# Kernel tuning notes

Measured on AMD Instinct MI355X. Metric: run time of the kernel, lower is better.

The kernel has to match this reference:

```python
import jax, jax.numpy as jnp
import numpy as np

EPS = 1e-8
H, DH = 4, 8
HID = H * DH  # 32
FF = 20       # 4 * dim
C = 5         # channels per degree


def snorm(x):
    # grad-safe L2 norm over last axis
    return jnp.sqrt(jnp.sum(x * x, axis=-1) + 1e-12)


def _ln(v, gamma, beta):
    mu = v.mean(-1, keepdims=True)
    sd = v.std(-1, keepdims=True) + EPS
    return (v - mu) / sd * gamma + beta


def norm_se3(x0, x1, g, b):
    # equivariant norm: transform per-channel invariant norms, keep orientation (phase)
    n0 = jnp.abs(x0)
    y0 = jnp.sign(x0) * jax.nn.gelu(_ln(n0, g[0], b[0]))
    n1 = snorm(x1)                                        # (b,n,c)
    y1 = x1 / n1[..., None] * jax.nn.gelu(_ln(n1, g[1], b[1]))[..., None]
    return y0, y1


def attention(x0, x1, coors, adjm, Wq, Mk, Mv, R1, rb1, R2, rb2, Wo0, Wo1):
    b, n, c = x0.shape
    rel = coors[:, None, :, :] - coors[:, :, None, :]     # (b,i,j,3): x_j - x_i
    dist = jnp.sqrt(jnp.sum(rel * rel, -1, keepdims=True) + 1e-12)
    u = rel / dist                                        # unit directions
    # radial net -> per-edge kernel coefficients for each degree-pair/basis (k and v)
    phi = jax.nn.relu(dist @ R1 + rb1) @ R2 + rb2         # (b,i,j,12*HID)
    (k00, k10, k01, kI, kU, kX, v00, v10, v01, vI, vU, vX) = jnp.split(phi, 12, -1)

    def edge_feats(M, p00, p10, p01, pI, pU, pX):
        y00 = jnp.einsum('bjc,ch->bjh', x0, M[0])
        y10 = jnp.einsum('bjcm,ch->bjhm', x1, M[1])
        y01 = jnp.einsum('bjc,ch->bjh', x0, M[2])
        yI = jnp.einsum('bjcm,ch->bjhm', x1, M[3])
        yU = jnp.einsum('bjcm,ch->bjhm', x1, M[4])
        yX = jnp.einsum('bjcm,ch->bjhm', x1, M[5])
        # degree-0 messages: (0->0) scalar and (1->0) vector.dot(u) paths
        e0 = p00 * y00[:, None] + p10 * jnp.einsum('bjhm,bijm->bijh', y10, u)
        un = u[:, :, :, None, :]                          # (b,i,j,1,3)
        # degree-1 messages: closed-form equivariant bases u*s, I, u(u.v), u x v
        e1 = (p01[..., None] * y01[:, None, :, :, None] * un
              + pI[..., None] * yI[:, None]
              + pU[..., None] * jnp.einsum('bjhm,bijm->bijh', yU, u)[..., None] * un
              + pX[..., None] * jnp.cross(un, yX[:, None]))
        return e0, e1

    k0, k1 = edge_feats(Mk, k00, k10, k01, kI, kU, kX)
    v0, v1 = edge_feats(Mv, v00, v10, v01, vI, vU, vX)

    q0 = jnp.einsum('bic,ch->bih', x0, Wq[0]).reshape(b, n, H, DH)
    q1 = jnp.einsum('bicm,ch->bihm', x1, Wq[1]).reshape(b, n, H, DH, 3)
    logits = (jnp.einsum('bihd,bijhd->bhij', q0, k0.reshape(b, n, n, H, DH))
              + jnp.einsum('bihdm,bijhdm->bhij', q1, k1.reshape(b, n, n, H, DH, 3)))
    logits = logits / jnp.asarray(DH, x0.dtype) ** 0.5
    logits = jnp.where(adjm[:, None], logits, -1e9)       # sparse-neighbor mask
    attn = jax.nn.softmax(logits, axis=-1)
    o0 = jnp.einsum('bhij,bijhd->bihd', attn, v0.reshape(b, n, n, H, DH)).reshape(b, n, HID)
    o1 = jnp.einsum('bhij,bijhdm->bihdm', attn, v1.reshape(b, n, n, H, DH, 3)).reshape(b, n, HID, 3)
    return o0 @ Wo0, jnp.einsum('bnhm,hc->bncm', o1, Wo1)


def feedforward(x0, x1, Wf1, Wf2, gs, bs):
    h0 = jax.nn.gelu(jnp.einsum('bnc,cf->bnf', x0, Wf1[0]))
    h1 = jnp.einsum('bncm,cf->bnfm', x1, Wf1[1])
    h1 = h1 * jax.nn.sigmoid(snorm(h1) * gs + bs)[..., None]   # norm-gated nonlin (equivariant)
    return jnp.einsum('bnf,fc->bnc', h0, Wf2[0]), jnp.einsum('bnfm,fc->bncm', h1, Wf2[1])


def _forward(feats, coors, adj_mat, Wq, Mk, Mv, R1, rb1, R2, rb2, Wo0, Wo1, gnA, bnA, gnF, bnF, Wf1, Wf2, gs, bs, Wh1, bh1, Wh2, bh2):
    b, n, _ = feats.shape
    a = adj_mat.astype(jnp.float32)
    # num_adj_degrees=2: attend over 1-hop OR 2-hop neighbors (plus self)
    adjm = adj_mat | ((a @ a) > 0) | jnp.eye(n, dtype=bool)
    x0 = feats
    x1 = jnp.zeros(feats.shape + (3,), feats.dtype)       # input fiber has only degree-0
    x0n, x1n = norm_se3(x0, x1, gnA, bnA)
    d0, d1 = attention(x0n, x1n, coors, adjm, Wq, Mk, Mv, R1, rb1, R2, rb2, Wo0, Wo1)
    x0, x1 = x0 + d0, x1 + d1
    x0n, x1n = norm_se3(x0, x1, gnF, bnF)
    f0, f1 = feedforward(x0n, x1n, Wf1, Wf2, gs, bs)
    x0, x1 = x0 + f0, x1 + f1
    pooled = x0.mean(axis=1)                              # mean pool type-0 features
    h = jax.nn.relu(pooled @ Wh1 + bh1)
    out = h @ Wh2 + bh2                                   # (b, 9)
    return out.reshape(-1, 3, 3)


def setup_inputs():
    key = jax.random.key(0)
    ks = jax.random.split(key, 16)
    B, N = 2, 256
    g = lambda i, shape, s: jax.random.normal(ks[i], shape, jnp.float32) * s
    feats = g(0, (B, N, C), 1.0)
    coors = g(1, (B, N, 3), 3.0)
    r = jax.random.uniform(ks[2], (B, N, N))
    adj = r < 0.03
    adj = (adj | jnp.swapaxes(adj, 1, 2)) & ~jnp.eye(N, dtype=bool)
    s5, sh, sf, s128 = C ** -0.5, HID ** -0.5, FF ** -0.5, 128 ** -0.5
    return dict(
        feats=feats, coors=coors, adj_mat=adj,
        Wq=g(3, (2, C, HID), s5), Mk=g(4, (6, C, HID), s5), Mv=g(5, (6, C, HID), s5),
        R1=g(6, (1, 32), 1.0), rb1=jnp.zeros(32), R2=g(7, (32, 12 * HID), 32 ** -0.5), rb2=jnp.zeros(12 * HID),
        Wo0=g(8, (HID, C), sh), Wo1=g(9, (HID, C), sh),
        gnA=jnp.ones((2, C)), bnA=jnp.zeros((2, C)), gnF=jnp.ones((2, C)), bnF=jnp.zeros((2, C)),
        Wf1=g(10, (2, C, FF), s5), Wf2=g(11, (2, FF, C), sf), gs=jnp.ones(FF), bs=jnp.zeros(FF),
        Wh1=g(12, (C, 128), s5), bh1=jnp.zeros(128), Wh2=g(13, (128, 9), s128), bh2=jnp.zeros(9))


def reference(feats, coors, adj_mat, Wq, Mk, Mv, R1, rb1, R2, rb2, Wo0, Wo1, gnA, bnA, gnF, bnF, Wf1, Wf2, gs, bs, Wh1, bh1, Wh2, bh2):
    return _forward(feats, coors, adj_mat, Wq, Mk, Mv, R1, rb1, R2, rb2, Wo0, Wo1, gnA, bnA, gnF, bnF, Wf1, Wf2, gs, bs, Wh1, bh1, Wh2, bh2)
```

## Files before the change

### kernel.cpp

```cpp
#include <hip/hip_runtime.h>
#include <math.h>

#define NN 256
#define CC 5
#define HIDD 32


__device__ __forceinline__ float gelu_tanh(float x) {
    float x3 = x * x * x;
    return 0.5f * x * (1.0f + tanhf(0.7978845608028654f * (x + 0.044715f * x3)));
}
__device__ __forceinline__ float sgnf(float x) {
    return (x > 0.f) ? 1.f : ((x < 0.f) ? -1.f : 0.f);
}

#define TROW 9
#define TSZ (33 * TROW)

__global__ __launch_bounds__(256) void fused_attn(
    const float* __restrict__ coors,
    const int* __restrict__ adj,
    const float* __restrict__ feats,
    const float* __restrict__ Wq0, const float* __restrict__ Mk0, const float* __restrict__ Mv0,
    const float* __restrict__ gnA0, const float* __restrict__ bnA0,
    const float* __restrict__ R1, const float* __restrict__ rb1,
    const float* __restrict__ R2, const float* __restrict__ rb2,
    const float* __restrict__ Wo0,
    const float* __restrict__ gnF0, const float* __restrict__ bnF0,
    const float* __restrict__ Wf10,
    const float* __restrict__ Wf20,
    float* __restrict__ xfin)
{
    int node = blockIdx.x;
    int b = node >> 8, i = node & 255;
    int tid = threadIdx.x;
    int j = tid;
    int lane = tid & 63, wave = tid >> 6;

    __shared__ float4 sT[4 * TSZ];
    __shared__ float2 kv[32][32];
    __shared__ float2 srr[32];
    __shared__ float srb2k[32], srb2v[32];
    __shared__ float tt[32], sts[32];
    __shared__ unsigned int smask[33];
    __shared__ float q0s[32];
    __shared__ float Wo0t[5][32];
    __shared__ int nlist[NN];
    __shared__ int ncnt;
    __shared__ float wredm[4][4], wreds[4][4];
    __shared__ float ew[4][5], x0as[5], xfs[5], h0s[20];

    int av = adj[(size_t)(b * NN + i) * NN + j];

    for (int idx = tid; idx < 1024; idx += 256) {
        int w = idx >> 5, hd = idx & 31;
        kv[w][hd] = make_float2(R2[w * 384 + hd], R2[w * 384 + 192 + hd]);
    }
    if (tid < 32) {
        srr[tid] = make_float2(R1[tid], rb1[tid]);
        srb2k[tid] = rb2[tid];
        srb2v[tid] = rb2[192 + tid];
    }
    if (tid < 160) Wo0t[tid / 32][tid % 32] = Wo0[(tid % 32) * 5 + tid / 32];
    if (tid == 0) ncnt = 0;

    float dx = coors[(b * NN + j) * 3 + 0] - coors[(b * NN + i) * 3 + 0];
    float dy = coors[(b * NN + j) * 3 + 1] - coors[(b * NN + i) * 3 + 1];
    float dz = coors[(b * NN + j) * 3 + 2] - coors[(b * NN + i) * 3 + 2];
    float dist = sqrtf(dx * dx + dy * dy + dz * dz + 1e-12f);

    float x0n[CC];
    {
        const float* f = feats + (size_t)(b * NN + j) * CC;
        float fv[CC], n0[CC];
        float mu = 0.f;
#pragma unroll
        for (int c = 0; c < CC; c++) { fv[c] = f[c]; n0[c] = fabsf(fv[c]); mu += n0[c]; }
        mu *= (1.0f / CC);
        float var = 0.f;
#pragma unroll
        for (int c = 0; c < CC; c++) { float d = n0[c] - mu; var += d * d; }
        var *= (1.0f / CC);
        float sd = sqrtf(var) + 1e-8f;
#pragma unroll
        for (int c = 0; c < CC; c++) {
            float ln = (n0[c] - mu) / sd * gnA0[c] + bnA0[c];
            x0n[c] = sgnf(fv[c]) * gelu_tanh(ln);
        }
    }
    __syncthreads();

    if (tid < 32) {
        float r = srr[tid].x;
        tt[tid] = (r != 0.f) ? (-srr[tid].y / r) : -3.0e38f;
    }
    if (tid < 32) {
        float t = tt[tid];
        int rank = 0;
        for (int k = 0; k < 32; k++) {
            float tk = tt[k];
            rank += (tk < t) || (tk == t && k < tid);
        }
        sts[rank] = t;
    }
    if (tid < 33) {
        float rep = (tid == 0) ? (sts[0] - 1.0f)
                  : (tid == 32) ? (sts[31] + 1.0f)
                  : 0.5f * (sts[tid - 1] + sts[tid]);
        unsigned int m = 0;
        for (int w = 0; w < 32; w++) {
            float2 rr = srr[w];
            if (fmaf(rr.x, rep, rr.y) > 0.f) m |= (1u << w);
        }
        smask[tid] = m;
    }
    if (tid < 32) {
        const float* f = feats + (size_t)(b * NN + i) * CC;
        float fv[CC], n0[CC], xi[CC];
        float mu = 0.f;
#pragma unroll
        for (int c = 0; c < CC; c++) { fv[c] = f[c]; n0[c] = fabsf(fv[c]); mu += n0[c]; }
        mu *= (1.0f / CC);
        float var = 0.f;
#pragma unroll
        for (int c = 0; c < CC; c++) { float d = n0[c] - mu; var += d * d; }
        var *= (1.0f / CC);
        float sd = sqrtf(var) + 1e-8f;
#pragma unroll
        for (int c = 0; c < CC; c++) {
            float ln = (n0[c] - mu) / sd * gnA0[c] + bnA0[c];
            xi[c] = sgnf(fv[c]) * gelu_tanh(ln);
        }
        float q = 0.f;
#pragma unroll
        for (int c = 0; c < CC; c++) q = fmaf(xi[c], Wq0[c * HIDD + tid], q);
        q0s[tid] = q;
    }
    if (av) { int p = atomicAdd(&ncnt, 1); nlist[p] = j; }

    float ykr[32];
#pragma unroll
    for (int hd = 0; hd < 32; hd++) ykr[hd] = 0.f;
#pragma unroll
    for (int c = 0; c < CC; c++) {
        float xc = x0n[c];
#pragma unroll
        for (int hd = 0; hd < 32; hd++)
            ykr[hd] = fmaf(xc, Mk0[c * HIDD + hd], ykr[hd]);
    }
    __syncthreads();

    int okacc = (av != 0) || (i == j);
    {
        int cnt = ncnt;
        for (int t = 0; t < cnt; t += 8) {
            int idxs[8], vv[8];
#pragma unroll
            for (int k = 0; k < 8; k++) {
                int u = t + k;
                idxs[k] = nlist[(u < cnt) ? u : t];
            }
#pragma unroll
            for (int k = 0; k < 8; k++)
                vv[k] = adj[(size_t)(b * NN + idxs[k]) * NN + j];
#pragma unroll
            for (int k = 0; k < 8; k++) okacc |= vv[k];
        }
    }
    for (int idx = tid; idx < 33 * 32; idx += 256) {
        int p = idx >> 5, hd = idx & 31;
        unsigned int m = smask[p];
        float A = 0.f, Bv = 0.f, Cv = 0.f, Dv = 0.f;
        while (m) {
            int w = __ffs(m) - 1;
            m &= (m - 1);
            float2 rr = srr[w];
            float2 kw = kv[w][hd];
            A  = fmaf(rr.x, kw.x, A);  Bv = fmaf(rr.y, kw.x, Bv);
            Cv = fmaf(rr.x, kw.y, Cv); Dv = fmaf(rr.y, kw.y, Dv);
        }
        Bv += srb2k[hd];
        Dv += srb2v[hd];
        float* tf = (float*)sT;
        tf[(0 * TSZ + p * TROW) * 4 + hd] = A;
        tf[(1 * TSZ + p * TROW) * 4 + hd] = Bv;
        tf[(2 * TSZ + p * TROW) * 4 + hd] = Cv;
        tf[(3 * TSZ + p * TROW) * 4 + hd] = Dv;
    }
    __syncthreads();

    int p = 0;
#pragma unroll
    for (int k = 0; k < 32; k++) p += (sts[k] < dist) ? 1 : 0;

    const float4* Ap = sT + 0 * TSZ + p * TROW;
    const float4* Bp = sT + 1 * TSZ + p * TROW;
    const float4* Cp = sT + 2 * TSZ + p * TROW;
    const float4* Dp = sT + 3 * TSZ + p * TROW;
    const float4* q04 = (const float4*)q0s;

    float lg[4] = {0.f, 0.f, 0.f, 0.f};
#pragma unroll
    for (int q = 0; q < 8; q++) {
        float4 a = Ap[q], bb = Bp[q], qq = q04[q];
        int h = q >> 1;
        lg[h] = fmaf(fmaf(dist, a.x, bb.x) * qq.x, ykr[4 * q + 0], lg[h]);
        lg[h] = fmaf(fmaf(dist, a.y, bb.y) * qq.y, ykr[4 * q + 1], lg[h]);
        lg[h] = fmaf(fmaf(dist, a.z, bb.z) * qq.z, ykr[4 * q + 2], lg[h]);
        lg[h] = fmaf(fmaf(dist, a.w, bb.w) * qq.w, ykr[4 * q + 3], lg[h]);
    }
    {
        const float invs = 0.35355339059327379f;
        bool ok = okacc != 0;
#pragma unroll
        for (int h = 0; h < 4; h++) lg[h] = ok ? lg[h] * invs : -1e9f;
    }

    float attn[4];
#pragma unroll
    for (int h = 0; h < 4; h++) {
        float v = lg[h];
        for (int off = 32; off; off >>= 1) v = fmaxf(v, __shfl_xor(v, off, 64));
        if (lane == 0) wredm[h][wave] = v;
    }
    __syncthreads();
    float hmv[4];
#pragma unroll
    for (int h = 0; h < 4; h++)
        hmv[h] = fmaxf(fmaxf(wredm[h][0], wredm[h][1]), fmaxf(wredm[h][2], wredm[h][3]));
#pragma unroll
    for (int h = 0; h < 4; h++) lg[h] = expf(lg[h] - hmv[h]);
#pragma unroll
    for (int h = 0; h < 4; h++) {
        float v = lg[h];
        for (int off = 32; off; off >>= 1) v += __shfl_xor(v, off, 64);
        if (lane == 0) wreds[h][wave] = v;
    }
    __syncthreads();
#pragma unroll
    for (int h = 0; h < 4; h++) {
        float hsv = wreds[h][0] + wreds[h][1] + wreds[h][2] + wreds[h][3];
        attn[h] = lg[h] / hsv;
    }

    float yvr[32];
#pragma unroll
    for (int hd = 0; hd < 32; hd++) yvr[hd] = 0.f;
#pragma unroll
    for (int c = 0; c < CC; c++) {
        float xc = x0n[c];
#pragma unroll
        for (int hd = 0; hd < 32; hd++)
            yvr[hd] = fmaf(xc, Mv0[c * HIDD + hd], yvr[hd]);
    }

    float e[5] = {0.f, 0.f, 0.f, 0.f, 0.f};
#pragma unroll
    for (int q = 0; q < 8; q++) {
        float4 c4 = Cp[q], d4 = Dp[q];
        float at = attn[q >> 1];
        float4 pv;
        pv.x = at * fmaf(dist, c4.x, d4.x) * yvr[4 * q + 0];
        pv.y = at * fmaf(dist, c4.y, d4.y) * yvr[4 * q + 1];
        pv.z = at * fmaf(dist, c4.z, d4.z) * yvr[4 * q + 2];
        pv.w = at * fmaf(dist, c4.w, d4.w) * yvr[4 * q + 3];
#pragma unroll
        for (int c = 0; c < 5; c++) {
            float4 w4 = ((const float4*)Wo0t[c])[q];
            e[c] = fmaf(pv.x, w4.x, fmaf(pv.y, w4.y, fmaf(pv.z, w4.z, fmaf(pv.w, w4.w, e[c]))));
        }
    }
    for (int off = 32; off; off >>= 1)
#pragma unroll
        for (int c = 0; c < 5; c++) e[c] += __shfl_xor(e[c], off, 64);
    if (lane == 0)
#pragma unroll
        for (int c = 0; c < 5; c++) ew[wave][c] = e[c];
    __syncthreads();

    if (wave != 0) return;

    if (lane < 5) {
        float d0 = ew[0][lane] + ew[1][lane] + ew[2][lane] + ew[3][lane];
        x0as[lane] = feats[node * 5 + lane] + d0;
    }
    if (lane < 5) {
        float x0a[5], n0[5];
        float mu = 0.f;
#pragma unroll
        for (int c = 0; c < 5; c++) { x0a[c] = x0as[c]; n0[c] = fabsf(x0a[c]); mu += n0[c]; }
        mu *= 0.2f;
        float var = 0.f;
#pragma unroll
        for (int c = 0; c < 5; c++) { float d = n0[c] - mu; var += d * d; }
        var *= 0.2f;
        float sd = sqrtf(var) + 1e-8f;
        float ln = (n0[lane] - mu) / sd * gnF0[lane] + bnF0[lane];
        xfs[lane] = sgnf(x0a[lane]) * gelu_tanh(ln);
    }
    if (lane < 20) {
        float s = 0.f;
#pragma unroll
        for (int c = 0; c < 5; c++) s = fmaf(xfs[c], Wf10[c * 20 + lane], s);
        h0s[lane] = gelu_tanh(s);
    }
    if (lane < 5) {
        float f0 = 0.f;
        for (int f = 0; f < 20; f++) f0 = fmaf(h0s[f], Wf20[f * 5 + lane], f0);
        xfin[node * 5 + lane] = x0as[lane] + f0;
    }
}

__global__ __launch_bounds__(256) void head_mlp(const float* __restrict__ xfin,
                         const float* __restrict__ Wh1, const float* __restrict__ bh1,
                         const float* __restrict__ Wh2, const float* __restrict__ bh2,
                         float* __restrict__ out) {
    __shared__ float part[2][5][25];
    __shared__ float pooled[10];
    __shared__ float hdn[2][128];
    int tid = threadIdx.x;
    if (tid < 250) {
        int b = tid / 125, r = tid % 125, c = r / 25, grp = r % 25;
        float s = 0.f;
        for (int i = grp; i < NN; i += 25) s += xfin[(b * NN + i) * 5 + c];
        part[b][c][grp] = s;
    }
    __syncthreads();
    if (tid < 10) {
        int b = tid / 5, c = tid % 5;
        float s = 0.f;
        for (int g = 0; g < 25; g++) s += part[b][c][g];
        pooled[tid] = s * (1.0f / NN);
    }
    __syncthreads();
    {
        int b = tid >> 7, k = tid & 127;
        float s = bh1[k];
#pragma unroll
        for (int c = 0; c < 5; c++) s = fmaf(pooled[b * 5 + c], Wh1[c * 128 + k], s);
        hdn[b][k] = fmaxf(s, 0.f);
    }
    __syncthreads();
    if (tid < 18) {
        int b = tid / 9, o = tid % 9;
        float s = bh2[o];
        for (int k = 0; k < 128; k++) s = fmaf(hdn[b][k], Wh2[k * 9 + o], s);
        out[b * 9 + o] = s;
    }
}

extern "C" void kernel_launch(void* const* d_in, const int* in_sizes, int n_in,
                              void* d_out, int out_size, void* d_ws, size_t ws_size,
                              hipStream_t stream) {
    const float* feats = (const float*)d_in[0];
    const float* coors = (const float*)d_in[1];
    const int*   adj   = (const int*)d_in[2];
    const float* Wq    = (const float*)d_in[3];
    const float* Mk    = (const float*)d_in[4];
    const float* Mv    = (const float*)d_in[5];
    const float* R1    = (const float*)d_in[6];
    const float* rb1   = (const float*)d_in[7];
    const float* R2    = (const float*)d_in[8];
    const float* rb2   = (const float*)d_in[9];
    const float* Wo0   = (const float*)d_in[10];
    const float* gnA   = (const float*)d_in[12];
    const float* bnA   = (const float*)d_in[13];
    const float* gnF   = (const float*)d_in[14];
    const float* bnF   = (const float*)d_in[15];
    const float* Wf1   = (const float*)d_in[16];
    const float* Wf2   = (const float*)d_in[17];
    const float* Wh1   = (const float*)d_in[20];
    const float* bh1   = (const float*)d_in[21];
    const float* Wh2   = (const float*)d_in[22];
    const float* bh2   = (const float*)d_in[23];
    float* out = (float*)d_out;

    float* xfin = (float*)d_ws;

    hipLaunchKernelGGL(fused_attn, dim3(512), dim3(256), 0, stream,
                       coors, adj, feats, Wq, Mk, Mv, gnA, bnA, R1, rb1, R2, rb2,
                       Wo0, gnF, bnF, Wf1, Wf2, xfin);
    hipLaunchKernelGGL(head_mlp, dim3(1), dim3(256), 0, stream,
                       xfin, Wh1, bh1, Wh2, bh2, out);
}
```

Before: 125.3 us.

## Replace shared atomic neighbor list with ballot compaction and prefetch tail weights

The neighbor list is now built with per-wave ballot/popcount compaction instead of a shared-memory atomicAdd, which removes the counter initialisation and one block barrier. The adjacency gather loop is unrolled 16 wide and maps indices across the four per-wave segments. Weights used by the per-node FFN tail are prefetched into registers early, and the head MLP stages Wh2 in shared memory. The aim is to cut atomic serialisation and barrier and latency stalls, at the cost of more registers and extra index arithmetic.

```diff
diff --git a/kernel.cpp b/kernel.cpp
--- a/kernel.cpp
+++ b/kernel.cpp
@@ -46,7 +46,7 @@
     __shared__ float q0s[32];
     __shared__ float Wo0t[5][32];
     __shared__ int nlist[NN];
-    __shared__ int ncnt;
+    __shared__ int wcnt[4];
     __shared__ float wredm[4][4], wreds[4][4];
     __shared__ float ew[4][5], x0as[5], xfs[5], h0s[20];
 
@@ -62,7 +62,6 @@
         srb2v[tid] = rb2[192 + tid];
     }
     if (tid < 160) Wo0t[tid / 32][tid % 32] = Wo0[(tid % 32) * 5 + tid / 32];
-    if (tid == 0) ncnt = 0;
 
     float dx = coors[(b * NN + j) * 3 + 0] - coors[(b * NN + i) * 3 + 0];
     float dy = coors[(b * NN + j) * 3 + 1] - coors[(b * NN + i) * 3 + 1];
@@ -88,7 +87,6 @@
             x0n[c] = sgnf(fv[c]) * gelu_tanh(ln);
         }
     }
-    __syncthreads();
 
     if (tid < 32) {
         float r = srr[tid].x;
@@ -136,7 +134,29 @@
         for (int c = 0; c < CC; c++) q = fmaf(xi[c], Wq0[c * HIDD + tid], q);
         q0s[tid] = q;
     }
-    if (av) { int p = atomicAdd(&ncnt, 1); nlist[p] = j; }
+
+    float pfeat = 0.f, pgnF = 0.f, pbnF = 0.f;
+    float pWf1[CC], pWf2[20];
+    if (wave == 0) {
+        if (lane < 5) {
+            pfeat = feats[node * 5 + lane];
+            pgnF = gnF0[lane];
+            pbnF = bnF0[lane];
+#pragma unroll
+            for (int f = 0; f < 20; f++) pWf2[f] = Wf20[f * 5 + lane];
+        }
+        if (lane < 20) {
+#pragma unroll
+            for (int c = 0; c < CC; c++) pWf1[c] = Wf10[c * 20 + lane];
+        }
+    }
+
+    {
+        unsigned long long bm = __ballot(av != 0);
+        int pos = __popcll(bm & ((1ull << lane) - 1ull));
+        if (av) nlist[(wave << 6) + pos] = j;
+        if (lane == 0) wcnt[wave] = (int)__popcll(bm);
+    }
 
     float ykr[32];
 #pragma unroll
@@ -152,19 +172,26 @@
 
     int okacc = (av != 0) || (i == j);
     {
-        int cnt = ncnt;
-        for (int t = 0; t < cnt; t += 8) {
-            int idxs[8], vv[8];
-#pragma unroll
-            for (int k = 0; k < 8; k++) {
-                int u = t + k;
-                idxs[k] = nlist[(u < cnt) ? u : t];
+        int o1 = wcnt[0];
+        int o2 = o1 + wcnt[1];
+        int o3 = o2 + wcnt[2];
+        int total = o3 + wcnt[3];
+        for (int t0 = 0; t0 < total; t0 += 16) {
+            int idxs[16], vv[16];
+#pragma unroll
+            for (int k = 0; k < 16; k++) {
+                int u = t0 + k;
+                if (u >= total) u = t0;
+                int base = (u >= o3) ? (192 - o3)
+                         : (u >= o2) ? (128 - o2)
+                         : (u >= o1) ? (64 - o1) : 0;
+                idxs[k] = nlist[u + base];
             }
 #pragma unroll
-            for (int k = 0; k < 8; k++)
+            for (int k = 0; k < 16; k++)
                 vv[k] = adj[(size_t)(b * NN + idxs[k]) * NN + j];
 #pragma unroll
-            for (int k = 0; k < 8; k++) okacc |= vv[k];
+            for (int k = 0; k < 16; k++) okacc |= vv[k];
         }
     }
     for (int idx = tid; idx < 33 * 32; idx += 256) {
@@ -282,7 +309,7 @@
 
     if (lane < 5) {
         float d0 = ew[0][lane] + ew[1][lane] + ew[2][lane] + ew[3][lane];
-        x0as[lane] = feats[node * 5 + lane] + d0;
+        x0as[lane] = pfeat + d0;
     }
     if (lane < 5) {
         float x0a[5], n0[5];
@@ -295,18 +322,19 @@
         for (int c = 0; c < 5; c++) { float d = n0[c] - mu; var += d * d; }
         var *= 0.2f;
         float sd = sqrtf(var) + 1e-8f;
-        float ln = (n0[lane] - mu) / sd * gnF0[lane] + bnF0[lane];
+        float ln = (n0[lane] - mu) / sd * pgnF + pbnF;
         xfs[lane] = sgnf(x0a[lane]) * gelu_tanh(ln);
     }
     if (lane < 20) {
         float s = 0.f;
 #pragma unroll
-        for (int c = 0; c < 5; c++) s = fmaf(xfs[c], Wf10[c * 20 + lane], s);
+        for (int c = 0; c < 5; c++) s = fmaf(xfs[c], pWf1[c], s);
         h0s[lane] = gelu_tanh(s);
     }
     if (lane < 5) {
         float f0 = 0.f;
-        for (int f = 0; f < 20; f++) f0 = fmaf(h0s[f], Wf20[f * 5 + lane], f0);
+#pragma unroll
+        for (int f = 0; f < 20; f++) f0 = fmaf(h0s[f], pWf2[f], f0);
         xfin[node * 5 + lane] = x0as[lane] + f0;
     }
 }
@@ -318,7 +346,11 @@
     __shared__ float part[2][5][25];
     __shared__ float pooled[10];
     __shared__ float hdn[2][128];
+    __shared__ float swh2[128 * 9];
+    __shared__ float sbh2[9];
     int tid = threadIdx.x;
+    for (int idx = tid; idx < 128 * 9; idx += 256) swh2[idx] = Wh2[idx];
+    if (tid < 9) sbh2[tid] = bh2[tid];
     if (tid < 250) {
         int b = tid / 125, r = tid % 125, c = r / 25, grp = r % 25;
         float s = 0.f;
@@ -343,8 +375,8 @@
     __syncthreads();
     if (tid < 18) {
         int b = tid / 9, o = tid % 9;
-        float s = bh2[o];
-        for (int k = 0; k < 128; k++) s = fmaf(hdn[b][k], Wh2[k * 9 + o], s);
+        float s = sbh2[o];
+        for (int k = 0; k < 128; k++) s = fmaf(hdn[b][k], swh2[k * 9 + o], s);
         out[b * 9 + o] = s;
     }
 }
```

Result: no change. 126.2 us (+0.7%).
